# Performance work log

Hardware: AMD Instinct MI355X
Metric: run time of the kernel (lower is better)

## Reference

```python
import jax, jax.numpy as jnp
import numpy as np

B, P, CD, RD, H, NR, OD, T = 1024, 22, 256, 64, 512, 12, 2, 100
IN = OD + 2 + CD + RD  # 324: [pos(2), ball(2), context(256), role_embed(64)]


def setup_inputs() -> dict:
    key = jax.random.key(0)
    ks = jax.random.split(key, 20)
    def n(k, shape, s=1.0):
        return jax.random.normal(k, shape, dtype=jnp.float32) * s
    sH = 1.0 / np.sqrt(H)
    sI = 1.0 / np.sqrt(IN)
    return {
        "context": n(ks[0], (B, P, CD)),
        "initial_position": n(ks[1], (B, P, OD)),
        "ball_landing": n(ks[2], (B, 2)),
        "roles": jax.random.randint(ks[3], (B, P), 0, NR, dtype=jnp.int32),
        "max_steps": T,
        "role_table": n(ks[4], (NR, RD), 0.02),
        # LSTM layer 0 (input_dim=IN)
        "W_ih0": n(ks[5], (4 * H, IN), sI),
        "W_hh0": n(ks[6], (4 * H, H), sH),
        "b0": n(ks[7], (4 * H,), sH),  # b_ih + b_hh fused
        # LSTM layer 1 (input_dim=H)
        "W_ih1": n(ks[8], (4 * H, H), sH),
        "W_hh1": n(ks[9], (4 * H, H), sH),
        "b1": n(ks[10], (4 * H,), sH),
        # output MLP: H -> H//2 -> OD
        "W_fc1": n(ks[11], (H // 2, H), sH),
        "b_fc1": n(ks[12], (H // 2,), sH),
        "W_fc2": n(ks[13], (OD, H // 2), 1.0 / np.sqrt(H // 2)),
        "b_fc2": n(ks[14], (OD,), 0.02),
        # initial_pos_encoder: Linear(OD, H)
        "W_init": n(ks[15], (H, OD), 1.0 / np.sqrt(OD)),
        "b_init": n(ks[16], (H,), 0.02),
    }


def _lstm_cell(x, h, c, W_ih, W_hh, b):
    # PyTorch gate order: i, f, g, o
    gates = x @ W_ih.T + h @ W_hh.T + b  # [N, 4H]
    i, f, g, o = jnp.split(gates, 4, axis=-1)
    c_new = jax.nn.sigmoid(f) * c + jax.nn.sigmoid(i) * jnp.tanh(g)
    h_new = jax.nn.sigmoid(o) * jnp.tanh(c_new)
    return h_new, c_new


def reference(context, initial_position, ball_landing, roles, max_steps,
              role_table, W_ih0, W_hh0, b0, W_ih1, W_hh1, b1,
              W_fc1, b_fc1, W_fc2, b_fc2, W_init, b_init):
    batch, num_players, context_dim = context.shape
    N = batch * num_players
    out_dim = initial_position.shape[-1]

    ctx_flat = context.reshape(N, context_dim)
    role_flat = role_table[roles].reshape(N, -1)
    ball_flat = jnp.broadcast_to(ball_landing[:, None, :], (batch, num_players, 2)).reshape(N, 2)
    static = jnp.concatenate([ball_flat, ctx_flat, role_flat], axis=1)  # [N, IN-2]

    pos0 = initial_position.reshape(N, out_dim)
    h0 = pos0 @ W_init.T + b_init  # initial_pos_encoder into layer-0 hidden
    c0 = jnp.zeros_like(h0)
    h1 = jnp.zeros_like(h0)
    c1 = jnp.zeros_like(h0)

    def step(carry, _):
        pos, h0, c0, h1, c1 = carry
        x = jnp.concatenate([pos, static], axis=1)  # [N, IN]
        h0, c0 = _lstm_cell(x, h0, c0, W_ih0, W_hh0, b0)
        h1, c1 = _lstm_cell(h0, h1, c1, W_ih1, W_hh1, b1)
        # output MLP (dropout inactive in eval)
        nxt = jax.nn.relu(h1 @ W_fc1.T + b_fc1) @ W_fc2.T + b_fc2  # [N, OD]
        return (nxt, h0, c0, h1, c1), nxt

    _, preds = jax.lax.scan(step, (pos0, h0, c0, h1, c1), None, length=max_steps)
    # preds: [T, N, OD] -> [batch, num_players, T, OD]
    preds = preds.transpose(1, 0, 2).reshape(batch, num_players, max_steps, out_dim)
    return preds
```

## Files before the change

kernel.cpp:

```cpp
#include <hip/hip_runtime.h>
#include <cstdint>


#define DEVI __device__ __forceinline__

typedef __bf16 bf16x8 __attribute__((ext_vector_type(8)));
typedef float  f32x4  __attribute__((ext_vector_type(4)));
typedef float  f32x2  __attribute__((ext_vector_type(2)));
typedef unsigned short u16x4 __attribute__((ext_vector_type(4)));

static constexpr int NROWS = 22528;
static constexpr int T_STEPS = 100;
static constexpr int NBM = 176;

DEVI unsigned short f2bf(float f) {
  unsigned u = __float_as_uint(f);
  u = u + 0x7FFFu + ((u >> 16) & 1u);
  return (unsigned short)(u >> 16);
}
DEVI float bf2f(unsigned short h) { return __uint_as_float(((unsigned)h) << 16); }

DEVI float fast_sigmoid(float x) {
  float e = __builtin_amdgcn_exp2f(-1.442695041f * x);
  return __builtin_amdgcn_rcpf(1.0f + e);
}
DEVI float fast_tanh(float x) {
  float e = __builtin_amdgcn_exp2f(2.885390082f * x);
  return 1.0f - 2.0f * __builtin_amdgcn_rcpf(e + 1.0f);
}

DEVI void async_copy16(const void* g, void* l) {
  __builtin_amdgcn_global_load_lds(
      (const __attribute__((address_space(1))) void*)g,
      (__attribute__((address_space(3))) void*)l, 16, 0, 0);
}

template <int KITERS, int KSWITCH>
DEVI void gemm_core(const unsigned short* __restrict__ A1, int lda1,
                    const unsigned short* __restrict__ A2, int lda2,
                    const unsigned short* __restrict__ B1, int ldb1,
                    const unsigned short* __restrict__ B2, int ldb2,
                    unsigned short* lds, f32x4 acc[4][4], int tid) {
  const int lane = tid & 63, wid = tid >> 6;
  const int wm = wid & 1, wn = wid >> 1;
  const int c16 = lane & 15, q = lane >> 4;
#pragma unroll
  for (int i = 0; i < 4; ++i)
#pragma unroll
    for (int j = 0; j < 4; ++j) acc[i][j] = f32x4{0.f, 0.f, 0.f, 0.f};
#pragma unroll
  for (int kt = 0; kt < KITERS; ++kt) {
    const bool sec = (kt >= KSWITCH);
    const unsigned short* Ab = sec ? A2 : A1;
    const unsigned short* Bb = sec ? B2 : B1;
    const int lda = sec ? lda2 : lda1;
    const int ldb = sec ? ldb2 : ldb1;
    const int kk = (sec ? (kt - KSWITCH) : kt) * 64;
    __syncthreads();
#pragma unroll
    for (int rd = 0; rd < 4; ++rd) {
      int p = rd * 256 + tid;
      int row = p >> 3, u = p & 7, ch = u ^ (row & 7);
      async_copy16(Ab + row * lda + kk + ch * 8, lds + p * 8);
      async_copy16(Bb + row * ldb + kk + ch * 8, lds + 8192 + p * 8);
    }
    __syncthreads();
#pragma unroll
    for (int s = 0; s < 2; ++s) {
      bf16x8 a[4], b[4];
#pragma unroll
      for (int mf = 0; mf < 4; ++mf) {
        int row = wm * 64 + mf * 16 + c16;
        int slot = row * 8 + ((s * 4 + q) ^ (row & 7));
        a[mf] = *(const bf16x8*)(lds + slot * 8);
      }
#pragma unroll
      for (int nf = 0; nf < 4; ++nf) {
        int row = wn * 64 + nf * 16 + c16;
        int slot = row * 8 + ((s * 4 + q) ^ (row & 7));
        b[nf] = *(const bf16x8*)(lds + 8192 + slot * 8);
      }
#pragma unroll
      for (int mf = 0; mf < 4; ++mf)
#pragma unroll
        for (int nf = 0; nf < 4; ++nf)
          acc[mf][nf] = __builtin_amdgcn_mfma_f32_16x16x32_bf16(a[mf], b[nf], acc[mf][nf], 0, 0, 0);
    }
  }
}

DEVI int orig_row(int j) {
  int tile = j >> 7, rem = j & 127;
  int half = rem >> 6, g = (rem >> 4) & 3, cc = rem & 15;
  return g * 512 + (tile * 32 + half * 16 + cc);
}

__global__ void k_prep_w(const float* __restrict__ Whh0, const float* __restrict__ Wih1,
                         const float* __restrict__ Whh1, const float* __restrict__ Wih0,
                         const float* __restrict__ Wfc1, const float* __restrict__ b0,
                         const float* __restrict__ b1,
                         unsigned short* __restrict__ W0p, unsigned short* __restrict__ Wc1p,
                         unsigned short* __restrict__ Wsp, unsigned short* __restrict__ Wfc1b,
                         float* __restrict__ Wposx, float* __restrict__ Wposy,
                         float* __restrict__ b0p4, float* __restrict__ b1p4) {
  int j = blockIdx.x;
  int k = threadIdx.x;
  int o = orig_row(j);
  W0p[j * 512 + k]         = f2bf(Whh0[o * 512 + k]);
  Wc1p[j * 1024 + k]       = f2bf(Wih1[o * 512 + k]);
  Wc1p[j * 1024 + 512 + k] = f2bf(Whh1[o * 512 + k]);
  if (k < 384) Wsp[j * 384 + k] = (k < 322) ? f2bf(Wih0[o * 324 + 2 + k]) : (unsigned short)0;
  if (k == 0) {
    int g = (j >> 4) & 3;
    int cg = (j >> 7) * 32 + ((j >> 6) & 1) * 16 + (j & 15);
    Wposx[cg * 4 + g] = Wih0[o * 324 + 0];
    Wposy[cg * 4 + g] = Wih0[o * 324 + 1];
    b0p4[cg * 4 + g] = b0[o];
    b1p4[cg * 4 + g] = b1[o];
  }
  if (j < 256) Wfc1b[j * 512 + k] = f2bf(Wfc1[j * 512 + k]);
}

__global__ void k_init_xs(const float* __restrict__ ball, const float* __restrict__ ctx,
                          const int* __restrict__ roles, const float* __restrict__ role_table,
                          unsigned short* __restrict__ Xs) {
  int n = blockIdx.x, col = threadIdx.x;
  int b = n / 22;
  float v;
  if (col < 2)        v = ball[b * 2 + col];
  else if (col < 258) v = ctx[(size_t)n * 256 + col - 2];
  else if (col < 322) v = role_table[roles[n] * 64 + col - 258];
  else                v = 0.f;
  Xs[(size_t)n * 384 + col] = f2bf(v);
}

__global__ void k_init_state(const float* __restrict__ pos0, const float* __restrict__ Winit,
                             const float* __restrict__ binit, unsigned short* __restrict__ Hcat,
                             float* __restrict__ c0, float* __restrict__ c1,
                             float* __restrict__ posb) {
  int idx = blockIdx.x * 256 + threadIdx.x;
  if (idx >= NROWS * 512) return;
  int n = idx >> 9, c = idx & 511;
  float px = pos0[n * 2 + 0], py = pos0[n * 2 + 1];
  float h0 = binit[c] + Winit[c * 2 + 0] * px + Winit[c * 2 + 1] * py;
  Hcat[(size_t)n * 1024 + c] = f2bf(h0);
  Hcat[(size_t)n * 1024 + 512 + c] = 0;
  c0[idx] = 0.f;
  c1[idx] = 0.f;
  if (c < 2) posb[n * 2 + c] = pos0[n * 2 + c];
}

__global__ __launch_bounds__(256) void k_static(const unsigned short* __restrict__ Xs,
                                                const unsigned short* __restrict__ Wsp,
                                                const float* __restrict__ b0p4,
                                                unsigned short* __restrict__ SP2) {
  __shared__ __align__(16) unsigned short lds[16384];
  int tid = threadIdx.x, bn = blockIdx.x, bm = blockIdx.y;
  f32x4 acc[4][4];
  const unsigned short* Ab = Xs + (size_t)bm * 128 * 384;
  const unsigned short* Bb = Wsp + (size_t)bn * 128 * 384;
  gemm_core<6, 6>(Ab, 384, Ab, 384, Bb, 384, Bb, 384, lds, acc, tid);
  int lane = tid & 63, wid = tid >> 6, wm = wid & 1, wn = wid >> 1;
  int c16 = lane & 15, q = lane >> 4;
  int cg = bn * 32 + wn * 16 + c16;
  f32x4 bb = *(const f32x4*)&b0p4[cg * 4];
#pragma unroll
  for (int mf = 0; mf < 4; ++mf) {
    int row0 = bm * 128 + wm * 64 + mf * 16 + q * 4;
#pragma unroll
    for (int r = 0; r < 4; ++r) {
      u16x4 v;
      v.x = f2bf(acc[mf][0][r] + bb.x);
      v.y = f2bf(acc[mf][1][r] + bb.y);
      v.z = f2bf(acc[mf][2][r] + bb.z);
      v.w = f2bf(acc[mf][3][r] + bb.w);
      ((u16x4*)SP2)[(size_t)(row0 + r) * 512 + cg] = v;
    }
  }
}


struct GemmSrc {
  const unsigned short *A1, *A2, *B1, *B2;
  int ldA1, ldA2, ldB1, ldB2;
};

template <int KT, int KSW>
DEVI void stage_q(const GemmSrc& g, int t, int s, int isB, unsigned short* dst, int tid) {
  int tt = (t >= KT) ? (t - 2) : t;
  const bool sec = (tt >= KSW);
  const unsigned short* base;
  int ld;
  if (isB) { base = sec ? g.B2 : g.B1; ld = sec ? g.ldB2 : g.ldB1; }
  else     { base = sec ? g.A2 : g.A1; ld = sec ? g.ldA2 : g.ldA1; }
  base += (sec ? (tt - KSW) : tt) * 64 + s * 32;
#pragma unroll
  for (int rd = 0; rd < 2; ++rd) {
    int p = rd * 512 + tid;
    int row = p >> 2, u = p & 3, ch = u ^ ((row >> 1) & 3);
    async_copy16(base + row * ld + ch * 8, dst + p * 8);
  }
}

#define GBAR   asm volatile("s_barrier" ::: "memory")
#define VMCNT4 asm volatile("s_waitcnt vmcnt(4)" ::: "memory")

template <int KT, int KSW>
DEVI void gemm8(const GemmSrc& g, unsigned short* lds, f32x4 acc[8][4], int tid) {
  const int lane = tid & 63, wid = tid >> 6;
  const int wm = wid >> 2, wn = wid & 3;
  const int c16 = lane & 15, q = lane >> 4;
#pragma unroll
  for (int i = 0; i < 8; ++i)
#pragma unroll
    for (int j = 0; j < 4; ++j) acc[i][j] = f32x4{0.f, 0.f, 0.f, 0.f};
  unsigned short* A00 = lds;
  unsigned short* A01 = lds + 8192;
  unsigned short* B00 = lds + 16384;
  unsigned short* B01 = lds + 24576;
  unsigned short* A10 = lds + 32768;
  unsigned short* A11 = lds + 40960;
  unsigned short* B10 = lds + 49152;
  unsigned short* B11 = lds + 57344;
  const int rowA0 = wm * 128 + c16;
  const int rowB0 = wn * 64 + c16;
  stage_q<KT, KSW>(g, 0, 0, 0, A00, tid);
  stage_q<KT, KSW>(g, 0, 0, 1, B00, tid);
  stage_q<KT, KSW>(g, 0, 1, 0, A01, tid);
  stage_q<KT, KSW>(g, 0, 1, 1, B01, tid);
  stage_q<KT, KSW>(g, 1, 0, 0, A10, tid);
  stage_q<KT, KSW>(g, 1, 0, 1, B10, tid);
  VMCNT4;
  GBAR;
  bf16x8 a[4], b[4];

#define LOADA(BASE, MG)                                                        \
  _Pragma("unroll")                                                            \
  for (int f = 0; f < 4; ++f) {                                                \
    int row = rowA0 + ((MG) * 4 + f) * 16;                                     \
    a[f] = *(const bf16x8*)((BASE) + (row * 4 + (q ^ ((row >> 1) & 3))) * 8);  \
  }
#define LOADB(BASE)                                                            \
  _Pragma("unroll")                                                            \
  for (int f = 0; f < 4; ++f) {                                                \
    int row = rowB0 + f * 16;                                                  \
    b[f] = *(const bf16x8*)((BASE) + (row * 4 + (q ^ ((row >> 1) & 3))) * 8);  \
  }
#define MFG(MG)                                                                \
  __builtin_amdgcn_s_setprio(1);                                               \
  _Pragma("unroll")                                                            \
  for (int f = 0; f < 4; ++f)                                                  \
    _Pragma("unroll")                                                          \
    for (int nf = 0; nf < 4; ++nf)                                             \
      acc[(MG) * 4 + f][nf] = __builtin_amdgcn_mfma_f32_16x16x32_bf16(         \
          a[f], b[nf], acc[(MG) * 4 + f][nf], 0, 0, 0);                        \
  __builtin_amdgcn_s_setprio(0);                                               \
  __builtin_amdgcn_sched_barrier(0);

#pragma unroll 1
  for (int it = 0; it < KT / 2; ++it) {
    const int t0 = 2 * it;
    LOADA(A00, 0); LOADB(B00);
    stage_q<KT, KSW>(g, t0 + 1, 1, 0, A11, tid);
    GBAR; MFG(0); GBAR;
    LOADA(A00, 1);
    stage_q<KT, KSW>(g, t0 + 1, 1, 1, B11, tid);
    GBAR; MFG(1); GBAR;
    LOADA(A01, 0); LOADB(B01);
    stage_q<KT, KSW>(g, t0 + 2, 0, 0, A00, tid);
    GBAR; MFG(0); GBAR;
    LOADA(A01, 1);
    stage_q<KT, KSW>(g, t0 + 2, 0, 1, B00, tid);
    GBAR; MFG(1); VMCNT4; GBAR;
    LOADA(A10, 0); LOADB(B10);
    stage_q<KT, KSW>(g, t0 + 2, 1, 0, A01, tid);
    GBAR; MFG(0); GBAR;
    LOADA(A10, 1);
    stage_q<KT, KSW>(g, t0 + 2, 1, 1, B01, tid);
    GBAR; MFG(1); GBAR;
    LOADA(A11, 0); LOADB(B11);
    stage_q<KT, KSW>(g, t0 + 3, 0, 0, A10, tid);
    GBAR; MFG(0); GBAR;
    LOADA(A11, 1);
    stage_q<KT, KSW>(g, t0 + 3, 0, 1, B10, tid);
    GBAR; MFG(1); VMCNT4; GBAR;
  }
  asm volatile("s_waitcnt vmcnt(0)" ::: "memory");
#undef LOADA
#undef LOADB
#undef MFG
}

DEVI void swz704(int l, int& bn, int& bm) {
  int xcd = l & 7, ii = l >> 3;
  bn = ii & 7;
  bm = (ii >> 3) * 8 + xcd;
}

template <bool USE_SP>
__global__ __launch_bounds__(512, 2) void k_s1_8(const unsigned short* __restrict__ cur,
                                                 const unsigned short* __restrict__ Xs,
                                                 const unsigned short* __restrict__ W0p,
                                                 const unsigned short* __restrict__ Wsp,
                                                 const unsigned short* __restrict__ SP2,
                                                 const float* __restrict__ b0p4,
                                                 const float* __restrict__ Wposx,
                                                 const float* __restrict__ Wposy,
                                                 const float* __restrict__ posb,
                                                 float* __restrict__ c0,
                                                 unsigned short* __restrict__ nxt) {
  __shared__ __align__(16) unsigned short lds[65536];
  const int tid = threadIdx.x;
  int bn, bm;
  swz704(blockIdx.x, bn, bm);
  f32x4 acc[8][4];
  GemmSrc g;
  g.A1 = cur + (size_t)bm * 256 * 1024; g.ldA1 = 1024;
  g.B1 = W0p + (size_t)bn * 256 * 512;  g.ldB1 = 512;
  if constexpr (USE_SP) {
    g.A2 = g.A1; g.ldA2 = 1024; g.B2 = g.B1; g.ldB2 = 512;
    gemm8<8, 8>(g, lds, acc, tid);
  } else {
    g.A2 = Xs + (size_t)bm * 256 * 384;  g.ldA2 = 384;
    g.B2 = Wsp + (size_t)bn * 256 * 384; g.ldB2 = 384;
    gemm8<14, 8>(g, lds, acc, tid);
  }
  const int lane = tid & 63, wid = tid >> 6;
  const int wm = wid >> 2, wn = wid & 3;
  const int c16 = lane & 15, q = lane >> 4;
  const int cg = bn * 64 + (wn >> 1) * 32 + (wn & 1) * 16 + c16;
  f32x4 wpx = *(const f32x4*)&Wposx[cg * 4];
  f32x4 wpy = *(const f32x4*)&Wposy[cg * 4];
  f32x4 sb = f32x4{0.f, 0.f, 0.f, 0.f};
  if constexpr (!USE_SP) sb = *(const f32x4*)&b0p4[cg * 4];
#pragma unroll
  for (int mf = 0; mf < 8; ++mf) {
    int row0 = bm * 256 + wm * 128 + mf * 16 + q * 4;
    f32x4 cold = *(const f32x4*)&c0[(size_t)cg * NROWS + row0];
    f32x4 cnew;
#pragma unroll
    for (int r = 0; r < 4; ++r) {
      size_t row = row0 + r;
      f32x2 pv = *(const f32x2*)&posb[row * 2];
      float s0 = sb.x, s1 = sb.y, s2 = sb.z, s3 = sb.w;
      if constexpr (USE_SP) {
        u16x4 sp = ((const u16x4*)SP2)[row * 512 + cg];
        s0 = bf2f(sp.x); s1 = bf2f(sp.y); s2 = bf2f(sp.z); s3 = bf2f(sp.w);
      }
      float gi = acc[mf][0][r] + s0 + pv.x * wpx.x + pv.y * wpy.x;
      float gf = acc[mf][1][r] + s1 + pv.x * wpx.y + pv.y * wpy.y;
      float gg = acc[mf][2][r] + s2 + pv.x * wpx.z + pv.y * wpy.z;
      float go = acc[mf][3][r] + s3 + pv.x * wpx.w + pv.y * wpy.w;
      float cn = fast_sigmoid(gf) * cold[r] + fast_sigmoid(gi) * fast_tanh(gg);
      cnew[r] = cn;
      nxt[row * 1024 + cg] = f2bf(fast_sigmoid(go) * fast_tanh(cn));
    }
    *(f32x4*)&c0[(size_t)cg * NROWS + row0] = cnew;
  }
}

__global__ __launch_bounds__(512, 2) void k_s2_8(const unsigned short* __restrict__ nxt_in,
                                                 const unsigned short* __restrict__ cur,
                                                 const unsigned short* __restrict__ Wc1p,
                                                 const float* __restrict__ b1p4,
                                                 float* __restrict__ c1,
                                                 unsigned short* __restrict__ nxt_out) {
  __shared__ __align__(16) unsigned short lds[65536];
  const int tid = threadIdx.x;
  int bn, bm;
  swz704(blockIdx.x, bn, bm);
  f32x4 acc[8][4];
  GemmSrc g;
  g.A1 = nxt_in + (size_t)bm * 256 * 1024;      g.ldA1 = 1024;
  g.A2 = cur + (size_t)bm * 256 * 1024 + 512;   g.ldA2 = 1024;
  g.B1 = Wc1p + (size_t)bn * 256 * 1024;        g.ldB1 = 1024;
  g.B2 = g.B1 + 512;                            g.ldB2 = 1024;
  gemm8<16, 8>(g, lds, acc, tid);
  const int lane = tid & 63, wid = tid >> 6;
  const int wm = wid >> 2, wn = wid & 3;
  const int c16 = lane & 15, q = lane >> 4;
  const int cg = bn * 64 + (wn >> 1) * 32 + (wn & 1) * 16 + c16;
  f32x4 bv = *(const f32x4*)&b1p4[cg * 4];
#pragma unroll
  for (int mf = 0; mf < 8; ++mf) {
    int row0 = bm * 256 + wm * 128 + mf * 16 + q * 4;
    f32x4 cold = *(const f32x4*)&c1[(size_t)cg * NROWS + row0];
    f32x4 cnew;
#pragma unroll
    for (int r = 0; r < 4; ++r) {
      size_t row = row0 + r;
      float gi = acc[mf][0][r] + bv.x;
      float gf = acc[mf][1][r] + bv.y;
      float gg = acc[mf][2][r] + bv.z;
      float go = acc[mf][3][r] + bv.w;
      float cn = fast_sigmoid(gf) * cold[r] + fast_sigmoid(gi) * fast_tanh(gg);
      cnew[r] = cn;
      nxt_out[row * 1024 + 512 + cg] = f2bf(fast_sigmoid(go) * fast_tanh(cn));
    }
    *(f32x4*)&c1[(size_t)cg * NROWS + row0] = cnew;
  }
}

__global__ __launch_bounds__(256) void k_s3(const unsigned short* __restrict__ H,
                                            const unsigned short* __restrict__ Wfc1b,
                                            const float* __restrict__ bfc1,
                                            const float* __restrict__ Wfc2,
                                            const float* __restrict__ bfc2,
                                            float* __restrict__ out, float* __restrict__ posb,
                                            int t) {
  __shared__ __align__(16) unsigned short ldsA[32 * 64];
  __shared__ __align__(16) unsigned short ldsB[256 * 64];
  __shared__ float wfc2s[512];
  __shared__ float red[32 * 8];
  int tid = threadIdx.x;
  int l = blockIdx.x, xcd = l & 7, i = l >> 3;
  int b32 = 4 * (xcd + 8 * (i >> 2)) + (i & 3);
  wfc2s[tid] = Wfc2[tid];
  wfc2s[tid + 256] = Wfc2[tid + 256];
  int lane = tid & 63, wid = tid >> 6;
  int c16 = lane & 15, q = lane >> 4;
  f32x4 acc[2][4];
#pragma unroll
  for (int ii = 0; ii < 2; ++ii)
#pragma unroll
    for (int jj = 0; jj < 4; ++jj) acc[ii][jj] = f32x4{0.f, 0.f, 0.f, 0.f};
  const unsigned short* Ab = H + (size_t)b32 * 32 * 1024 + 512;
#pragma unroll
  for (int kt = 0; kt < 8; ++kt) {
    int k0 = kt * 64;
    __syncthreads();
    {
      int p = tid;
      int row = p >> 3, u = p & 7, ch = u ^ (row & 7);
      async_copy16(Ab + row * 1024 + k0 + ch * 8, ldsA + p * 8);
    }
#pragma unroll
    for (int rd = 0; rd < 8; ++rd) {
      int p = rd * 256 + tid;
      int row = p >> 3, u = p & 7, ch = u ^ (row & 7);
      async_copy16(Wfc1b + row * 512 + k0 + ch * 8, ldsB + p * 8);
    }
    __syncthreads();
#pragma unroll
    for (int s = 0; s < 2; ++s) {
      bf16x8 a[2], b[4];
#pragma unroll
      for (int mf = 0; mf < 2; ++mf) {
        int row = mf * 16 + c16;
        int slot = row * 8 + ((s * 4 + q) ^ (row & 7));
        a[mf] = *(const bf16x8*)(ldsA + slot * 8);
      }
#pragma unroll
      for (int nf = 0; nf < 4; ++nf) {
        int row = wid * 64 + nf * 16 + c16;
        int slot = row * 8 + ((s * 4 + q) ^ (row & 7));
        b[nf] = *(const bf16x8*)(ldsB + slot * 8);
      }
#pragma unroll
      for (int mf = 0; mf < 2; ++mf)
#pragma unroll
        for (int nf = 0; nf < 4; ++nf)
          acc[mf][nf] = __builtin_amdgcn_mfma_f32_16x16x32_bf16(a[mf], b[nf], acc[mf][nf], 0, 0, 0);
    }
  }
  float part[2][2][4];
#pragma unroll
  for (int d = 0; d < 2; ++d)
#pragma unroll
    for (int mf = 0; mf < 2; ++mf)
#pragma unroll
      for (int r = 0; r < 4; ++r) part[d][mf][r] = 0.f;
#pragma unroll
  for (int nf = 0; nf < 4; ++nf) {
    int col = wid * 64 + nf * 16 + c16;
    float w0 = wfc2s[col], w1 = wfc2s[256 + col], bv = bfc1[col];
#pragma unroll
    for (int mf = 0; mf < 2; ++mf)
#pragma unroll
      for (int r = 0; r < 4; ++r) {
        float v = acc[mf][nf][r] + bv;
        v = v > 0.f ? v : 0.f;
        part[0][mf][r] += v * w0;
        part[1][mf][r] += v * w1;
      }
  }
#pragma unroll
  for (int st = 1; st < 16; st <<= 1)
#pragma unroll
    for (int d = 0; d < 2; ++d)
#pragma unroll
      for (int mf = 0; mf < 2; ++mf)
#pragma unroll
        for (int r = 0; r < 4; ++r)
          part[d][mf][r] += __shfl_xor(part[d][mf][r], st, 64);
  if (c16 == 0) {
#pragma unroll
    for (int mf = 0; mf < 2; ++mf)
#pragma unroll
      for (int r = 0; r < 4; ++r) {
        int rl = mf * 16 + q * 4 + r;
        red[rl * 8 + wid * 2 + 0] = part[0][mf][r];
        red[rl * 8 + wid * 2 + 1] = part[1][mf][r];
      }
  }
  __syncthreads();
  if (tid < 64) {
    int rl = tid >> 1, d = tid & 1;
    float s = red[rl * 8 + d] + red[rl * 8 + 2 + d] + red[rl * 8 + 4 + d]
            + red[rl * 8 + 6 + d] + bfc2[d];
    int rg = b32 * 32 + rl;
    out[((size_t)rg * T_STEPS + t) * 2 + d] = s;
    posb[rg * 2 + d] = s;
  }
}

extern "C" void kernel_launch(void* const* d_in, const int* in_sizes, int n_in,
                              void* d_out, int out_size, void* d_ws, size_t ws_size,
                              hipStream_t stream) {
  (void)in_sizes; (void)n_in; (void)out_size;
  const float* ctx   = (const float*)d_in[0];
  const float* pos0  = (const float*)d_in[1];
  const float* ball  = (const float*)d_in[2];
  const int*   roles = (const int*)d_in[3];
  const float* role_table = (const float*)d_in[5];
  const float* Wih0 = (const float*)d_in[6];
  const float* Whh0 = (const float*)d_in[7];
  const float* b0   = (const float*)d_in[8];
  const float* Wih1 = (const float*)d_in[9];
  const float* Whh1 = (const float*)d_in[10];
  const float* b1   = (const float*)d_in[11];
  const float* Wfc1 = (const float*)d_in[12];
  const float* bfc1 = (const float*)d_in[13];
  const float* Wfc2 = (const float*)d_in[14];
  const float* bfc2 = (const float*)d_in[15];
  const float* Winit = (const float*)d_in[16];
  const float* binit = (const float*)d_in[17];
  float* out = (float*)d_out;

  char* w = (char*)d_ws;
  size_t used = 0;
  auto alloc = [&](size_t bytes) {
    char* p = w + used;
    used += (bytes + 255) & ~(size_t)255;
    return p;
  };
  unsigned short* W0p   = (unsigned short*)alloc((size_t)2048 * 512 * 2);
  unsigned short* Wc1p  = (unsigned short*)alloc((size_t)2048 * 1024 * 2);
  unsigned short* Wfc1b = (unsigned short*)alloc((size_t)256 * 512 * 2);
  float* Wposx = (float*)alloc(2048 * 4);
  float* Wposy = (float*)alloc(2048 * 4);
  float* b0p4  = (float*)alloc(2048 * 4);
  float* b1p4  = (float*)alloc(2048 * 4);
  float* posb  = (float*)alloc((size_t)NROWS * 2 * 4);
  unsigned short* Hc0 = (unsigned short*)alloc((size_t)NROWS * 1024 * 2);
  float* c0   = (float*)alloc((size_t)NROWS * 512 * 4);
  float* c1   = (float*)alloc((size_t)NROWS * 512 * 4);
  unsigned short* Hc1 = (unsigned short*)alloc((size_t)NROWS * 1024 * 2);

  const size_t SP_BYTES = (size_t)NROWS * 2048 * 2;
  const bool use_sp = (ws_size >= used + SP_BYTES + (1u << 20));

  unsigned short *Xs, *Wsp, *SP2;
  if (use_sp) {
    SP2 = (unsigned short*)alloc(SP_BYTES);
    Xs  = Hc1;
    Wsp = Hc1 + (size_t)NROWS * 384;
  } else {
    SP2 = Hc1;
    Xs  = (unsigned short*)alloc((size_t)NROWS * 384 * 2);
    Wsp = (unsigned short*)alloc((size_t)2048 * 384 * 2);
  }

  k_prep_w<<<2048, 512, 0, stream>>>(Whh0, Wih1, Whh1, Wih0, Wfc1, b0, b1,
                                     W0p, Wc1p, Wsp, Wfc1b, Wposx, Wposy, b0p4, b1p4);
  k_init_xs<<<NROWS, 384, 0, stream>>>(ball, ctx, roles, role_table, Xs);
  k_init_state<<<(NROWS * 512 + 255) / 256, 256, 0, stream>>>(pos0, Winit, binit, Hc0, c0, c1, posb);

  if (use_sp) {
    dim3 gs(16, NBM);
    k_static<<<gs, 256, 0, stream>>>(Xs, Wsp, b0p4, SP2);
  }

  for (int t = 0; t < T_STEPS; ++t) {
    unsigned short* cur = (t & 1) ? Hc1 : Hc0;
    unsigned short* nxt = (t & 1) ? Hc0 : Hc1;
    if (use_sp)
      k_s1_8<true><<<704, 512, 0, stream>>>(cur, Xs, W0p, Wsp, SP2, b0p4,
                                            Wposx, Wposy, posb, c0, nxt);
    else
      k_s1_8<false><<<704, 512, 0, stream>>>(cur, Xs, W0p, Wsp, SP2, b0p4,
                                             Wposx, Wposy, posb, c0, nxt);
    k_s2_8<<<704, 512, 0, stream>>>(nxt, cur, Wc1p, b1p4, c1, nxt);
    k_s3<<<704, 256, 0, stream>>>(nxt, Wfc1b, bfc1, Wfc2, bfc2, out, posb, t);
  }
}
```

Baseline: 21.78 ms.

## Fuse per-step LSTM stages into one launch with per-row-block flag synchronization

Merges the three per-timestep kernels (layer-0 cell, layer-1 cell, output MLP) into a single launch of 1760 blocks. Block ranges are assigned to each stage, and release/acquire atomic counters per 256-row block order the stages. Downstream blocks start as soon as their row block's producers finish, rather than waiting on a full kernel boundary. This removes two launches and tail drains per step. In exchange, waiting blocks spin and occupy CU slots, and correctness relies on blocks being dispatched roughly in order.

```diff
diff --git a/kernel.cpp b/kernel.cpp
--- a/kernel.cpp
+++ b/kernel.cpp
@@ -137,7 +137,9 @@
 __global__ void k_init_state(const float* __restrict__ pos0, const float* __restrict__ Winit,
                              const float* __restrict__ binit, unsigned short* __restrict__ Hcat,
                              float* __restrict__ c0, float* __restrict__ c1,
-                             float* __restrict__ posb) {
+                             float* __restrict__ posb,
+                             unsigned int* __restrict__ done0,
+                             unsigned int* __restrict__ done1) {
   int idx = blockIdx.x * 256 + threadIdx.x;
   if (idx >= NROWS * 512) return;
   int n = idx >> 9, c = idx & 511;
@@ -148,6 +150,7 @@
   c0[idx] = 0.f;
   c1[idx] = 0.f;
   if (c < 2) posb[n * 2 + c] = pos0[n * 2 + c];
+  if (idx < 88) { done0[idx] = 0u; done1[idx] = 0u; }
 }
 
 __global__ __launch_bounds__(256) void k_static(const unsigned short* __restrict__ Xs,
@@ -178,7 +181,6 @@
     }
   }
 }
-
 
 struct GemmSrc {
   const unsigned short *A1, *A2, *B1, *B2;
@@ -298,219 +300,230 @@
 }
 
 template <bool USE_SP>
-__global__ __launch_bounds__(512, 2) void k_s1_8(const unsigned short* __restrict__ cur,
-                                                 const unsigned short* __restrict__ Xs,
-                                                 const unsigned short* __restrict__ W0p,
-                                                 const unsigned short* __restrict__ Wsp,
-                                                 const unsigned short* __restrict__ SP2,
-                                                 const float* __restrict__ b0p4,
-                                                 const float* __restrict__ Wposx,
-                                                 const float* __restrict__ Wposy,
-                                                 const float* __restrict__ posb,
-                                                 float* __restrict__ c0,
-                                                 unsigned short* __restrict__ nxt) {
+__global__ __launch_bounds__(512, 2) void k_step(
+    const unsigned short* __restrict__ cur, unsigned short* __restrict__ nxt,
+    const unsigned short* __restrict__ Xs,
+    const unsigned short* __restrict__ W0p, const unsigned short* __restrict__ Wsp,
+    const unsigned short* __restrict__ SP2, const float* __restrict__ b0p4,
+    const float* __restrict__ Wposx, const float* __restrict__ Wposy,
+    float* __restrict__ posb, float* __restrict__ c0,
+    const unsigned short* __restrict__ Wc1p, const float* __restrict__ b1p4,
+    float* __restrict__ c1,
+    const unsigned short* __restrict__ Wfc1b, const float* __restrict__ bfc1,
+    const float* __restrict__ Wfc2, const float* __restrict__ bfc2,
+    float* __restrict__ out, unsigned int* __restrict__ done0,
+    unsigned int* __restrict__ done1, int t) {
   __shared__ __align__(16) unsigned short lds[65536];
   const int tid = threadIdx.x;
-  int bn, bm;
-  swz704(blockIdx.x, bn, bm);
-  f32x4 acc[8][4];
-  GemmSrc g;
-  g.A1 = cur + (size_t)bm * 256 * 1024; g.ldA1 = 1024;
-  g.B1 = W0p + (size_t)bn * 256 * 512;  g.ldB1 = 512;
-  if constexpr (USE_SP) {
-    g.A2 = g.A1; g.ldA2 = 1024; g.B2 = g.B1; g.ldB2 = 512;
-    gemm8<8, 8>(g, lds, acc, tid);
+  const int bid = blockIdx.x;
+  const unsigned thr = 8u * (unsigned)(t + 1);
+
+  if (bid < 704) {
+    int bn, bm;
+    swz704(bid, bn, bm);
+    f32x4 acc[8][4];
+    GemmSrc g;
+    g.A1 = cur + (size_t)bm * 256 * 1024; g.ldA1 = 1024;
+    g.B1 = W0p + (size_t)bn * 256 * 512;  g.ldB1 = 512;
+    if constexpr (USE_SP) {
+      g.A2 = g.A1; g.ldA2 = 1024; g.B2 = g.B1; g.ldB2 = 512;
+      gemm8<8, 8>(g, lds, acc, tid);
+    } else {
+      g.A2 = Xs + (size_t)bm * 256 * 384;  g.ldA2 = 384;
+      g.B2 = Wsp + (size_t)bn * 256 * 384; g.ldB2 = 384;
+      gemm8<14, 8>(g, lds, acc, tid);
+    }
+    const int lane = tid & 63, wid = tid >> 6;
+    const int wm = wid >> 2, wn = wid & 3;
+    const int c16 = lane & 15, q = lane >> 4;
+    const int cg = bn * 64 + (wn >> 1) * 32 + (wn & 1) * 16 + c16;
+    f32x4 wpx = *(const f32x4*)&Wposx[cg * 4];
+    f32x4 wpy = *(const f32x4*)&Wposy[cg * 4];
+    f32x4 sb = f32x4{0.f, 0.f, 0.f, 0.f};
+    if constexpr (!USE_SP) sb = *(const f32x4*)&b0p4[cg * 4];
+#pragma unroll
+    for (int mf = 0; mf < 8; ++mf) {
+      int row0 = bm * 256 + wm * 128 + mf * 16 + q * 4;
+      f32x4 cold = *(const f32x4*)&c0[(size_t)cg * NROWS + row0];
+      f32x4 cnew;
+#pragma unroll
+      for (int r = 0; r < 4; ++r) {
+        size_t row = row0 + r;
+        f32x2 pv = *(const f32x2*)&posb[row * 2];
+        float s0 = sb.x, s1 = sb.y, s2 = sb.z, s3 = sb.w;
+        if constexpr (USE_SP) {
+          u16x4 sp = ((const u16x4*)SP2)[row * 512 + cg];
+          s0 = bf2f(sp.x); s1 = bf2f(sp.y); s2 = bf2f(sp.z); s3 = bf2f(sp.w);
+        }
+        float gi = acc[mf][0][r] + s0 + pv.x * wpx.x + pv.y * wpy.x;
+        float gf = acc[mf][1][r] + s1 + pv.x * wpx.y + pv.y * wpy.y;
+        float gg = acc[mf][2][r] + s2 + pv.x * wpx.z + pv.y * wpy.z;
+        float go = acc[mf][3][r] + s3 + pv.x * wpx.w + pv.y * wpy.w;
+        float cn = fast_sigmoid(gf) * cold[r] + fast_sigmoid(gi) * fast_tanh(gg);
+        cnew[r] = cn;
+        nxt[row * 1024 + cg] = f2bf(fast_sigmoid(go) * fast_tanh(cn));
+      }
+      *(f32x4*)&c0[(size_t)cg * NROWS + row0] = cnew;
+    }
+    __threadfence();
+    __syncthreads();
+    if (tid == 0)
+      __hip_atomic_fetch_add(&done0[bm], 1u, __ATOMIC_RELEASE, __HIP_MEMORY_SCOPE_AGENT);
+  } else if (bid < 1408) {
+    int bn, bm;
+    swz704(bid - 704, bn, bm);
+    if (tid == 0) {
+      while (__hip_atomic_load(&done0[bm], __ATOMIC_ACQUIRE, __HIP_MEMORY_SCOPE_AGENT) < thr)
+        __builtin_amdgcn_s_sleep(2);
+    }
+    __syncthreads();
+    __builtin_amdgcn_fence(__ATOMIC_ACQUIRE, "agent");
+    f32x4 acc[8][4];
+    GemmSrc g;
+    g.A1 = nxt + (size_t)bm * 256 * 1024;         g.ldA1 = 1024;
+    g.A2 = cur + (size_t)bm * 256 * 1024 + 512;   g.ldA2 = 1024;
+    g.B1 = Wc1p + (size_t)bn * 256 * 1024;        g.ldB1 = 1024;
+    g.B2 = g.B1 + 512;                            g.ldB2 = 1024;
+    gemm8<16, 8>(g, lds, acc, tid);
+    const int lane = tid & 63, wid = tid >> 6;
+    const int wm = wid >> 2, wn = wid & 3;
+    const int c16 = lane & 15, q = lane >> 4;
+    const int cg = bn * 64 + (wn >> 1) * 32 + (wn & 1) * 16 + c16;
+    f32x4 bv = *(const f32x4*)&b1p4[cg * 4];
+#pragma unroll
+    for (int mf = 0; mf < 8; ++mf) {
+      int row0 = bm * 256 + wm * 128 + mf * 16 + q * 4;
+      f32x4 cold = *(const f32x4*)&c1[(size_t)cg * NROWS + row0];
+      f32x4 cnew;
+#pragma unroll
+      for (int r = 0; r < 4; ++r) {
+        size_t row = row0 + r;
+        float gi = acc[mf][0][r] + bv.x;
+        float gf = acc[mf][1][r] + bv.y;
+        float gg = acc[mf][2][r] + bv.z;
+        float go = acc[mf][3][r] + bv.w;
+        float cn = fast_sigmoid(gf) * cold[r] + fast_sigmoid(gi) * fast_tanh(gg);
+        cnew[r] = cn;
+        nxt[row * 1024 + 512 + cg] = f2bf(fast_sigmoid(go) * fast_tanh(cn));
+      }
+      *(f32x4*)&c1[(size_t)cg * NROWS + row0] = cnew;
+    }
+    __threadfence();
+    __syncthreads();
+    if (tid == 0)
+      __hip_atomic_fetch_add(&done1[bm], 1u, __ATOMIC_RELEASE, __HIP_MEMORY_SCOPE_AGENT);
   } else {
-    g.A2 = Xs + (size_t)bm * 256 * 384;  g.ldA2 = 384;
-    g.B2 = Wsp + (size_t)bn * 256 * 384; g.ldB2 = 384;
-    gemm8<14, 8>(g, lds, acc, tid);
-  }
-  const int lane = tid & 63, wid = tid >> 6;
-  const int wm = wid >> 2, wn = wid & 3;
-  const int c16 = lane & 15, q = lane >> 4;
-  const int cg = bn * 64 + (wn >> 1) * 32 + (wn & 1) * 16 + c16;
-  f32x4 wpx = *(const f32x4*)&Wposx[cg * 4];
-  f32x4 wpy = *(const f32x4*)&Wposy[cg * 4];
-  f32x4 sb = f32x4{0.f, 0.f, 0.f, 0.f};
-  if constexpr (!USE_SP) sb = *(const f32x4*)&b0p4[cg * 4];
-#pragma unroll
-  for (int mf = 0; mf < 8; ++mf) {
-    int row0 = bm * 256 + wm * 128 + mf * 16 + q * 4;
-    f32x4 cold = *(const f32x4*)&c0[(size_t)cg * NROWS + row0];
-    f32x4 cnew;
-#pragma unroll
-    for (int r = 0; r < 4; ++r) {
-      size_t row = row0 + r;
-      f32x2 pv = *(const f32x2*)&posb[row * 2];
-      float s0 = sb.x, s1 = sb.y, s2 = sb.z, s3 = sb.w;
-      if constexpr (USE_SP) {
-        u16x4 sp = ((const u16x4*)SP2)[row * 512 + cg];
-        s0 = bf2f(sp.x); s1 = bf2f(sp.y); s2 = bf2f(sp.z); s3 = bf2f(sp.w);
+    const int s = bid - 1408;
+    const int inst = tid >> 8, t256 = tid & 255;
+    const int b32 = 2 * s + inst;
+    if (tid == 0) {
+      while (__hip_atomic_load(&done1[b32 >> 3], __ATOMIC_ACQUIRE, __HIP_MEMORY_SCOPE_AGENT) < thr)
+        __builtin_amdgcn_s_sleep(2);
+    }
+    __syncthreads();
+    __builtin_amdgcn_fence(__ATOMIC_ACQUIRE, "agent");
+    unsigned short* ldsI = lds + inst * 32768;
+    unsigned short* ldsA = ldsI;
+    unsigned short* ldsB = ldsI + 2048;
+    float* wfc2s = (float*)(ldsI + 2048 + 16384);
+    float* red   = wfc2s + 512;
+    wfc2s[t256] = Wfc2[t256];
+    wfc2s[t256 + 256] = Wfc2[t256 + 256];
+    int lane = t256 & 63, wid = t256 >> 6;
+    int c16 = lane & 15, q = lane >> 4;
+    f32x4 acc[2][4];
+#pragma unroll
+    for (int ii = 0; ii < 2; ++ii)
+#pragma unroll
+      for (int jj = 0; jj < 4; ++jj) acc[ii][jj] = f32x4{0.f, 0.f, 0.f, 0.f};
+    const unsigned short* Ab = nxt + (size_t)b32 * 32 * 1024 + 512;
+#pragma unroll
+    for (int kt = 0; kt < 8; ++kt) {
+      int k0 = kt * 64;
+      __syncthreads();
+      {
+        int p = t256;
+        int row = p >> 3, u = p & 7, ch = u ^ (row & 7);
+        async_copy16(Ab + row * 1024 + k0 + ch * 8, ldsA + p * 8);
       }
-      float gi = acc[mf][0][r] + s0 + pv.x * wpx.x + pv.y * wpy.x;
-      float gf = acc[mf][1][r] + s1 + pv.x * wpx.y + pv.y * wpy.y;
-      float gg = acc[mf][2][r] + s2 + pv.x * wpx.z + pv.y * wpy.z;
-      float go = acc[mf][3][r] + s3 + pv.x * wpx.w + pv.y * wpy.w;
-      float cn = fast_sigmoid(gf) * cold[r] + fast_sigmoid(gi) * fast_tanh(gg);
-      cnew[r] = cn;
-      nxt[row * 1024 + cg] = f2bf(fast_sigmoid(go) * fast_tanh(cn));
-    }
-    *(f32x4*)&c0[(size_t)cg * NROWS + row0] = cnew;
-  }
-}
-
-__global__ __launch_bounds__(512, 2) void k_s2_8(const unsigned short* __restrict__ nxt_in,
-                                                 const unsigned short* __restrict__ cur,
-                                                 const unsigned short* __restrict__ Wc1p,
-                                                 const float* __restrict__ b1p4,
-                                                 float* __restrict__ c1,
-                                                 unsigned short* __restrict__ nxt_out) {
-  __shared__ __align__(16) unsigned short lds[65536];
-  const int tid = threadIdx.x;
-  int bn, bm;
-  swz704(blockIdx.x, bn, bm);
-  f32x4 acc[8][4];
-  GemmSrc g;
-  g.A1 = nxt_in + (size_t)bm * 256 * 1024;      g.ldA1 = 1024;
-  g.A2 = cur + (size_t)bm * 256 * 1024 + 512;   g.ldA2 = 1024;
-  g.B1 = Wc1p + (size_t)bn * 256 * 1024;        g.ldB1 = 1024;
-  g.B2 = g.B1 + 512;                            g.ldB2 = 1024;
-  gemm8<16, 8>(g, lds, acc, tid);
-  const int lane = tid & 63, wid = tid >> 6;
-  const int wm = wid >> 2, wn = wid & 3;
-  const int c16 = lane & 15, q = lane >> 4;
-  const int cg = bn * 64 + (wn >> 1) * 32 + (wn & 1) * 16 + c16;
-  f32x4 bv = *(const f32x4*)&b1p4[cg * 4];
-#pragma unroll
-  for (int mf = 0; mf < 8; ++mf) {
-    int row0 = bm * 256 + wm * 128 + mf * 16 + q * 4;
-    f32x4 cold = *(const f32x4*)&c1[(size_t)cg * NROWS + row0];
-    f32x4 cnew;
-#pragma unroll
-    for (int r = 0; r < 4; ++r) {
-      size_t row = row0 + r;
-      float gi = acc[mf][0][r] + bv.x;
-      float gf = acc[mf][1][r] + bv.y;
-      float gg = acc[mf][2][r] + bv.z;
-      float go = acc[mf][3][r] + bv.w;
-      float cn = fast_sigmoid(gf) * cold[r] + fast_sigmoid(gi) * fast_tanh(gg);
-      cnew[r] = cn;
-      nxt_out[row * 1024 + 512 + cg] = f2bf(fast_sigmoid(go) * fast_tanh(cn));
-    }
-    *(f32x4*)&c1[(size_t)cg * NROWS + row0] = cnew;
-  }
-}
-
-__global__ __launch_bounds__(256) void k_s3(const unsigned short* __restrict__ H,
-                                            const unsigned short* __restrict__ Wfc1b,
-                                            const float* __restrict__ bfc1,
-                                            const float* __restrict__ Wfc2,
-                                            const float* __restrict__ bfc2,
-                                            float* __restrict__ out, float* __restrict__ posb,
-                                            int t) {
-  __shared__ __align__(16) unsigned short ldsA[32 * 64];
-  __shared__ __align__(16) unsigned short ldsB[256 * 64];
-  __shared__ float wfc2s[512];
-  __shared__ float red[32 * 8];
-  int tid = threadIdx.x;
-  int l = blockIdx.x, xcd = l & 7, i = l >> 3;
-  int b32 = 4 * (xcd + 8 * (i >> 2)) + (i & 3);
-  wfc2s[tid] = Wfc2[tid];
-  wfc2s[tid + 256] = Wfc2[tid + 256];
-  int lane = tid & 63, wid = tid >> 6;
-  int c16 = lane & 15, q = lane >> 4;
-  f32x4 acc[2][4];
-#pragma unroll
-  for (int ii = 0; ii < 2; ++ii)
-#pragma unroll
-    for (int jj = 0; jj < 4; ++jj) acc[ii][jj] = f32x4{0.f, 0.f, 0.f, 0.f};
-  const unsigned short* Ab = H + (size_t)b32 * 32 * 1024 + 512;
-#pragma unroll
-  for (int kt = 0; kt < 8; ++kt) {
-    int k0 = kt * 64;
+#pragma unroll
+      for (int rd = 0; rd < 8; ++rd) {
+        int p = rd * 256 + t256;
+        int row = p >> 3, u = p & 7, ch = u ^ (row & 7);
+        async_copy16(Wfc1b + row * 512 + k0 + ch * 8, ldsB + p * 8);
+      }
+      __syncthreads();
+#pragma unroll
+      for (int ss = 0; ss < 2; ++ss) {
+        bf16x8 a[2], b[4];
+#pragma unroll
+        for (int mf = 0; mf < 2; ++mf) {
+          int row = mf * 16 + c16;
+          int slot = row * 8 + ((ss * 4 + q) ^ (row & 7));
+          a[mf] = *(const bf16x8*)(ldsA + slot * 8);
+        }
+#pragma unroll
+        for (int nf = 0; nf < 4; ++nf) {
+          int row = wid * 64 + nf * 16 + c16;
+          int slot = row * 8 + ((ss * 4 + q) ^ (row & 7));
+          b[nf] = *(const bf16x8*)(ldsB + slot * 8);
+        }
+#pragma unroll
+        for (int mf = 0; mf < 2; ++mf)
+#pragma unroll
+          for (int nf = 0; nf < 4; ++nf)
+            acc[mf][nf] = __builtin_amdgcn_mfma_f32_16x16x32_bf16(a[mf], b[nf], acc[mf][nf], 0, 0, 0);
+      }
+    }
+    float part[2][2][4];
+#pragma unroll
+    for (int d = 0; d < 2; ++d)
+#pragma unroll
+      for (int mf = 0; mf < 2; ++mf)
+#pragma unroll
+        for (int r = 0; r < 4; ++r) part[d][mf][r] = 0.f;
+#pragma unroll
+    for (int nf = 0; nf < 4; ++nf) {
+      int col = wid * 64 + nf * 16 + c16;
+      float w0 = wfc2s[col], w1 = wfc2s[256 + col], bv = bfc1[col];
+#pragma unroll
+      for (int mf = 0; mf < 2; ++mf)
+#pragma unroll
+        for (int r = 0; r < 4; ++r) {
+          float v = acc[mf][nf][r] + bv;
+          v = v > 0.f ? v : 0.f;
+          part[0][mf][r] += v * w0;
+          part[1][mf][r] += v * w1;
+        }
+    }
+#pragma unroll
+    for (int st = 1; st < 16; st <<= 1)
+#pragma unroll
+      for (int d = 0; d < 2; ++d)
+#pragma unroll
+        for (int mf = 0; mf < 2; ++mf)
+#pragma unroll
+          for (int r = 0; r < 4; ++r)
+            part[d][mf][r] += __shfl_xor(part[d][mf][r], st, 64);
+    if (c16 == 0) {
+#pragma unroll
+      for (int mf = 0; mf < 2; ++mf)
+#pragma unroll
+        for (int r = 0; r < 4; ++r) {
+          int rl = mf * 16 + q * 4 + r;
+          red[rl * 8 + wid * 2 + 0] = part[0][mf][r];
+          red[rl * 8 + wid * 2 + 1] = part[1][mf][r];
+        }
+    }
     __syncthreads();
-    {
-      int p = tid;
-      int row = p >> 3, u = p & 7, ch = u ^ (row & 7);
-      async_copy16(Ab + row * 1024 + k0 + ch * 8, ldsA + p * 8);
-    }
-#pragma unroll
-    for (int rd = 0; rd < 8; ++rd) {
-      int p = rd * 256 + tid;
-      int row = p >> 3, u = p & 7, ch = u ^ (row & 7);
-      async_copy16(Wfc1b + row * 512 + k0 + ch * 8, ldsB + p * 8);
-    }
-    __syncthreads();
-#pragma unroll
-    for (int s = 0; s < 2; ++s) {
-      bf16x8 a[2], b[4];
-#pragma unroll
-      for (int mf = 0; mf < 2; ++mf) {
-        int row = mf * 16 + c16;
-        int slot = row * 8 + ((s * 4 + q) ^ (row & 7));
-        a[mf] = *(const bf16x8*)(ldsA + slot * 8);
-      }
-#pragma unroll
-      for (int nf = 0; nf < 4; ++nf) {
-        int row = wid * 64 + nf * 16 + c16;
-        int slot = row * 8 + ((s * 4 + q) ^ (row & 7));
-        b[nf] = *(const bf16x8*)(ldsB + slot * 8);
-      }
-#pragma unroll
-      for (int mf = 0; mf < 2; ++mf)
-#pragma unroll
-        for (int nf = 0; nf < 4; ++nf)
-          acc[mf][nf] = __builtin_amdgcn_mfma_f32_16x16x32_bf16(a[mf], b[nf], acc[mf][nf], 0, 0, 0);
-    }
-  }
-  float part[2][2][4];
-#pragma unroll
-  for (int d = 0; d < 2; ++d)
-#pragma unroll
-    for (int mf = 0; mf < 2; ++mf)
-#pragma unroll
-      for (int r = 0; r < 4; ++r) part[d][mf][r] = 0.f;
-#pragma unroll
-  for (int nf = 0; nf < 4; ++nf) {
-    int col = wid * 64 + nf * 16 + c16;
-    float w0 = wfc2s[col], w1 = wfc2s[256 + col], bv = bfc1[col];
-#pragma unroll
-    for (int mf = 0; mf < 2; ++mf)
-#pragma unroll
-      for (int r = 0; r < 4; ++r) {
-        float v = acc[mf][nf][r] + bv;
-        v = v > 0.f ? v : 0.f;
-        part[0][mf][r] += v * w0;
-        part[1][mf][r] += v * w1;
-      }
-  }
-#pragma unroll
-  for (int st = 1; st < 16; st <<= 1)
-#pragma unroll
-    for (int d = 0; d < 2; ++d)
-#pragma unroll
-      for (int mf = 0; mf < 2; ++mf)
-#pragma unroll
-        for (int r = 0; r < 4; ++r)
-          part[d][mf][r] += __shfl_xor(part[d][mf][r], st, 64);
-  if (c16 == 0) {
-#pragma unroll
-    for (int mf = 0; mf < 2; ++mf)
-#pragma unroll
-      for (int r = 0; r < 4; ++r) {
-        int rl = mf * 16 + q * 4 + r;
-        red[rl * 8 + wid * 2 + 0] = part[0][mf][r];
-        red[rl * 8 + wid * 2 + 1] = part[1][mf][r];
-      }
-  }
-  __syncthreads();
-  if (tid < 64) {
-    int rl = tid >> 1, d = tid & 1;
-    float s = red[rl * 8 + d] + red[rl * 8 + 2 + d] + red[rl * 8 + 4 + d]
-            + red[rl * 8 + 6 + d] + bfc2[d];
-    int rg = b32 * 32 + rl;
-    out[((size_t)rg * T_STEPS + t) * 2 + d] = s;
-    posb[rg * 2 + d] = s;
+    if (t256 < 64) {
+      int rl = t256 >> 1, d = t256 & 1;
+      float sum = red[rl * 8 + d] + red[rl * 8 + 2 + d] + red[rl * 8 + 4 + d]
+                + red[rl * 8 + 6 + d] + bfc2[d];
+      int rg = b32 * 32 + rl;
+      out[((size_t)rg * T_STEPS + t) * 2 + d] = sum;
+      posb[rg * 2 + d] = sum;
+    }
   }
 }
 
@@ -552,6 +565,8 @@
   float* b0p4  = (float*)alloc(2048 * 4);
   float* b1p4  = (float*)alloc(2048 * 4);
   float* posb  = (float*)alloc((size_t)NROWS * 2 * 4);
+  unsigned int* done0 = (unsigned int*)alloc(88 * 4);
+  unsigned int* done1 = (unsigned int*)alloc(88 * 4);
   unsigned short* Hc0 = (unsigned short*)alloc((size_t)NROWS * 1024 * 2);
   float* c0   = (float*)alloc((size_t)NROWS * 512 * 4);
   float* c1   = (float*)alloc((size_t)NROWS * 512 * 4);
@@ -574,7 +589,8 @@
   k_prep_w<<<2048, 512, 0, stream>>>(Whh0, Wih1, Whh1, Wih0, Wfc1, b0, b1,
                                      W0p, Wc1p, Wsp, Wfc1b, Wposx, Wposy, b0p4, b1p4);
   k_init_xs<<<NROWS, 384, 0, stream>>>(ball, ctx, roles, role_table, Xs);
-  k_init_state<<<(NROWS * 512 + 255) / 256, 256, 0, stream>>>(pos0, Winit, binit, Hc0, c0, c1, posb);
+  k_init_state<<<(NROWS * 512 + 255) / 256, 256, 0, stream>>>(pos0, Winit, binit, Hc0,
+                                                              c0, c1, posb, done0, done1);
 
   if (use_sp) {
     dim3 gs(16, NBM);
@@ -585,12 +601,14 @@
     unsigned short* cur = (t & 1) ? Hc1 : Hc0;
     unsigned short* nxt = (t & 1) ? Hc0 : Hc1;
     if (use_sp)
-      k_s1_8<true><<<704, 512, 0, stream>>>(cur, Xs, W0p, Wsp, SP2, b0p4,
-                                            Wposx, Wposy, posb, c0, nxt);
+      k_step<true><<<1760, 512, 0, stream>>>(cur, nxt, Xs, W0p, Wsp, SP2, b0p4,
+                                             Wposx, Wposy, posb, c0, Wc1p, b1p4, c1,
+                                             Wfc1b, bfc1, Wfc2, bfc2, out,
+                                             done0, done1, t);
     else
-      k_s1_8<false><<<704, 512, 0, stream>>>(cur, Xs, W0p, Wsp, SP2, b0p4,
-                                             Wposx, Wposy, posb, c0, nxt);
-    k_s2_8<<<704, 512, 0, stream>>>(nxt, cur, Wc1p, b1p4, c1, nxt);
-    k_s3<<<704, 256, 0, stream>>>(nxt, Wfc1b, bfc1, Wfc2, bfc2, out, posb, t);
-  }
-}
+      k_step<false><<<1760, 512, 0, stream>>>(cur, nxt, Xs, W0p, Wsp, SP2, b0p4,
+                                              Wposx, Wposy, posb, c0, Wc1p, b1p4, c1,
+                                              Wfc1b, bfc1, Wfc2, bfc2, out,
+                                              done0, done1, t);
+  }
+}
```

After: 71.49 ms. 228% more time.
